# Kernel optimization log

Measured on AMD Instinct MI355X. Metric: run time of the kernel, lower is better.

Reference implementation:

```python
import jax, jax.numpy as jnp
import numpy as np

NUM_CLASSES = 10
PGD_NUMS = 10
ALPHA = 0.15
# Hardcoded in the original module: sign vector for 10 classes
SIGN_VEC = jnp.array([-1.0] * 4 + [1.0] * 6, dtype=jnp.float32)


def setup_inputs() -> dict:
    key = jax.random.key(0)
    k1, k2, k3 = jax.random.split(key, 3)
    B = 1048576
    logit = jax.random.normal(k1, (B, NUM_CLASSES), dtype=jnp.float32)
    y = jax.random.randint(k2, (B,), 0, NUM_CLASSES, dtype=jnp.int32)
    label_freq = jax.random.randint(k3, (NUM_CLASSES,), 0, PGD_NUMS, dtype=jnp.int32)
    return {"logit": logit, "y": y, "label_freq": label_freq}


def _compute_adv(logit, y):
    # softmax over classes, then per-class mean of softmax rows (one-hot^T @ p)
    p = jax.nn.softmax(logit, axis=-1)  # [B, C]
    sum_class_logit = jax.ops.segment_sum(p, y, num_segments=NUM_CLASSES)  # [C, C]
    counts = jax.ops.segment_sum(jnp.ones(y.shape[0], dtype=logit.dtype), y,
                                 num_segments=NUM_CLASSES)  # [C]
    counts = jnp.where(counts == 0, jnp.asarray(100.0, logit.dtype), counts)
    mean_class_logit = sum_class_logit / counts[:, None]  # [C, C]
    grad = mean_class_logit - jnp.eye(NUM_CLASSES, dtype=logit.dtype)
    # Faithful to torch: norm over dim=0 (columns), then reshape(-1,1) divides row i
    col_norm = jnp.linalg.norm(grad, axis=0)  # [C]
    grad = grad / col_norm[:, None]
    grad = ALPHA * grad * SIGN_VEC[:, None].astype(logit.dtype)
    return grad[y]  # index_select along dim 0 -> [B, C]


def reference(logit, y, label_freq):
    logit_copy = logit

    def step(l, _):
        l_new = l + _compute_adv(l, y)
        return l_new, l_new

    _, logit_steps = jax.lax.scan(step, logit, None, length=PGD_NUMS)  # [P, B, C]

    # Original: logit_news = sum_i logit_steps[label_freq[i]] * (y == i)
    # Since class masks are disjoint, this is a per-sample gather of step label_freq[y[n]].
    steps_per_sample = label_freq[y]  # [B]
    B = logit.shape[0]
    logit_news = logit_steps[steps_per_sample, jnp.arange(B)]  # [B, C]

    # mean cross-entropy
    log_p = jax.nn.log_softmax(logit_news, axis=-1)
    loss_adv = -jnp.mean(jnp.take_along_axis(log_p, y[:, None].astype(jnp.int32), axis=1))
    return loss_adv, logit_news, logit_copy
```

## Files before the change

### kernel.cpp

```cpp
#include <hip/hip_runtime.h>

#define PGD   10
#define ALPHA 0.15f
#define NTAB  32
#define NTHR  256
#define SPT   4
#define FTHR  256
#define FSPT  4

#define WS_COUNTS 0
#define WS_STAB   320
#define WS_DGLOB  32320
#define WS_ZERO_N 33320

__global__ void k_init(float* __restrict__ ws, float* __restrict__ out) {
    int i = blockIdx.x * blockDim.x + threadIdx.x;
    if (i == 0) out[0] = 0.f;
    int gs = gridDim.x * blockDim.x;
    for (int k = i; k < WS_ZERO_N; k += gs) ws[k] = 0.f;
}

__device__ __forceinline__ void load4(const float* __restrict__ logit,
                                      const int* __restrict__ y,
                                      int s0, int B, float a[40], int yc[4]) {
    if (s0 + 4 <= B) {
        const float4* rp = reinterpret_cast<const float4*>(logit + (size_t)s0 * 10);
        float4 q[10];
        #pragma unroll
        for (int i = 0; i < 10; ++i) q[i] = rp[i];
        int4 yv = *reinterpret_cast<const int4*>(y + s0);
        #pragma unroll
        for (int i = 0; i < 10; ++i) {
            a[4 * i + 0] = q[i].x; a[4 * i + 1] = q[i].y;
            a[4 * i + 2] = q[i].z; a[4 * i + 3] = q[i].w;
        }
        yc[0] = yv.x; yc[1] = yv.y; yc[2] = yv.z; yc[3] = yv.w;
    } else {
        #pragma unroll
        for (int k = 0; k < 4; ++k) {
            int idx = s0 + k;
            if (idx < B) {
                yc[k] = y[idx];
                for (int j = 0; j < 10; ++j) a[k * 10 + j] = logit[(size_t)idx * 10 + j];
            } else {
                yc[k] = -1;
                for (int j = 0; j < 10; ++j) a[k * 10 + j] = 0.f;
            }
        }
    }
}

__global__ __launch_bounds__(NTHR) void k_step(
    const float* __restrict__ logit, const int* __restrict__ y,
    float* __restrict__ ws, int B, int t )
{
    __shared__ float sh_D[100];
    __shared__ float shT[100];
    __shared__ float shCnt[10];
    __shared__ float shCn[10];
    __shared__ float wtab[8][100];
    __shared__ float ctab[8][10];

    const int tid = threadIdx.x;

    float* counts_tab = ws + WS_COUNTS;
    float* S_tab      = ws + WS_STAB;
    float* D_glob     = ws + WS_DGLOB;

    for (int i = tid; i < 800; i += NTHR) (&wtab[0][0])[i] = 0.f;
    if (t == 1) for (int i = tid; i < 80; i += NTHR) (&ctab[0][0])[i] = 0.f;

    if (t >= 2) {
        const float* Sg = S_tab + (size_t)(t - 2) * (NTAB * 100);
        if (tid < 10) {
            float s = 0.f;
            #pragma unroll
            for (int k = 0; k < NTAB; ++k) s += counts_tab[k * 10 + tid];
            shCnt[tid] = (s == 0.f) ? 100.f : s;
        }
        if (tid < 100) {
            float s = 0.f;
            #pragma unroll
            for (int k = 0; k < NTAB; ++k) s += Sg[k * 100 + tid];
            shT[tid] = s;
        }
        __syncthreads();
        if (tid < 100) {
            int c = tid / 10, j = tid - c * 10;
            shT[tid] = shT[tid] / shCnt[c] - ((c == j) ? 1.f : 0.f);
        }
        __syncthreads();
        if (tid < 10) {
            float s = 0.f;
            for (int cc = 0; cc < 10; ++cc) { float g = shT[cc * 10 + tid]; s += g * g; }
            shCn[tid] = sqrtf(s);
        }
        __syncthreads();
        if (tid < 100) {
            int c = tid / 10;
            float sign = (c < 4) ? -1.f : 1.f;
            float g = shT[tid] / shCn[c] * (ALPHA * sign);
            sh_D[tid] = ((t >= 3) ? D_glob[(size_t)(t - 3) * 100 + tid] : 0.f) + g;
        }
        __syncthreads();
        if (blockIdx.x == 0 && tid < 100) D_glob[(size_t)(t - 2) * 100 + tid] = sh_D[tid];
    }
    __syncthreads();

    const int s0 = (blockIdx.x * NTHR + tid) * SPT;
    float a[40];
    int   yc[4];
    load4(logit, y, s0, B, a, yc);

    const int sub = ((tid >> 6) << 1) | (tid & 1);
    #pragma unroll
    for (int k = 0; k < SPT; ++k) {
        int c = yc[k];
        if (c < 0) continue;
        float tv[10];
        #pragma unroll
        for (int j = 0; j < 10; ++j) tv[j] = a[k * 10 + j];
        if (t >= 2) {
            #pragma unroll
            for (int j = 0; j < 10; ++j) tv[j] += sh_D[c * 10 + j];
        }
        float m = tv[0];
        #pragma unroll
        for (int j = 1; j < 10; ++j) m = fmaxf(m, tv[j]);
        float s = 0.f;
        #pragma unroll
        for (int j = 0; j < 10; ++j) { tv[j] = __expf(tv[j] - m); s += tv[j]; }
        float r = 1.f / s;
        #pragma unroll
        for (int j = 0; j < 10; ++j) unsafeAtomicAdd(&wtab[sub][c * 10 + j], tv[j] * r);
        if (t == 1) unsafeAtomicAdd(&ctab[sub][c], 1.f);
    }
    __syncthreads();

    const int tb = blockIdx.x & (NTAB - 1);
    if (tid < 100) {
        float s = 0.f;
        #pragma unroll
        for (int w = 0; w < 8; ++w) s += wtab[w][tid];
        unsafeAtomicAdd(&S_tab[(size_t)(t - 1) * (NTAB * 100) + (size_t)tb * 100 + tid], s);
    }
    if (t == 1 && tid < 10) {
        float s = 0.f;
        #pragma unroll
        for (int w = 0; w < 8; ++w) s += ctab[w][tid];
        unsafeAtomicAdd(&counts_tab[tb * 10 + tid], s);
    }
}

__global__ __launch_bounds__(FTHR) void k_final(
    const float* __restrict__ logit, const int* __restrict__ y,
    const int* __restrict__ label_freq,
    float* __restrict__ out, float* __restrict__ ws, int B)
{
    __shared__ float Dall[PGD][100];
    __shared__ float shT[100];
    __shared__ float shCnt[10];
    __shared__ float shCn[10];
    __shared__ int   lf[10];
    __shared__ float wsum[4];

    const int tid = threadIdx.x;

    float* counts_tab = ws + WS_COUNTS;
    float* S_tab      = ws + WS_STAB;
    float* D_glob     = ws + WS_DGLOB;

    {
        const float* Sg = S_tab + (size_t)9 * (NTAB * 100);
        if (tid < 10) {
            float s = 0.f;
            #pragma unroll
            for (int k = 0; k < NTAB; ++k) s += counts_tab[k * 10 + tid];
            shCnt[tid] = (s == 0.f) ? 100.f : s;
        }
        if (tid < 100) {
            float s = 0.f;
            #pragma unroll
            for (int k = 0; k < NTAB; ++k) s += Sg[k * 100 + tid];
            shT[tid] = s;
        }
        __syncthreads();
        if (tid < 100) {
            int c = tid / 10, j = tid - c * 10;
            shT[tid] = shT[tid] / shCnt[c] - ((c == j) ? 1.f : 0.f);
        }
        __syncthreads();
        if (tid < 10) {
            float s = 0.f;
            for (int cc = 0; cc < 10; ++cc) { float g = shT[cc * 10 + tid]; s += g * g; }
            shCn[tid] = sqrtf(s);
        }
        __syncthreads();
        if (tid < 100) {
            int c = tid / 10;
            float sign = (c < 4) ? -1.f : 1.f;
            float g = shT[tid] / shCn[c] * (ALPHA * sign);
            Dall[9][tid] = D_glob[8 * 100 + tid] + g;
        }
        for (int i = tid; i < 900; i += FTHR) Dall[i / 100][i % 100] = D_glob[i];
        if (tid < 10) lf[tid] = label_freq[tid];
        __syncthreads();
    }

    const int s0 = (blockIdx.x * FTHR + tid) * FSPT;
    float a[40];
    int   yc[4];
    load4(logit, y, s0, B, a, yc);

    float* news_out = out + 1;
    float* copy_out = out + 1 + (size_t)B * 10;
    float acc = 0.f;
    #pragma unroll
    for (int k = 0; k < FSPT; ++k) {
        int idx = s0 + k;
        if (idx >= B || yc[k] < 0) continue;
        int c = yc[k];
        int sel = lf[c];
        float nv[10];
        #pragma unroll
        for (int j = 0; j < 10; ++j) nv[j] = a[k * 10 + j] + Dall[sel][c * 10 + j];
        float2* np = reinterpret_cast<float2*>(news_out + (size_t)idx * 10);
        float2* cp = reinterpret_cast<float2*>(copy_out + (size_t)idx * 10);
        #pragma unroll
        for (int q = 0; q < 5; ++q) {
            np[q] = make_float2(nv[2 * q], nv[2 * q + 1]);
            cp[q] = make_float2(a[k * 10 + 2 * q], a[k * 10 + 2 * q + 1]);
        }
        float m = nv[0];
        #pragma unroll
        for (int j = 1; j < 10; ++j) m = fmaxf(m, nv[j]);
        float s = 0.f;
        #pragma unroll
        for (int j = 0; j < 10; ++j) s += __expf(nv[j] - m);
        acc += __logf(s) + m - nv[c];
    }
    #pragma unroll
    for (int off = 32; off > 0; off >>= 1) acc += __shfl_down(acc, off);
    if ((tid & 63) == 0) wsum[tid >> 6] = acc;
    __syncthreads();
    if (tid == 0)
        unsafeAtomicAdd(out, (wsum[0] + wsum[1] + wsum[2] + wsum[3]) / (float)B);
}

extern "C" void kernel_launch(void* const* d_in, const int* in_sizes, int n_in,
                              void* d_out, int out_size, void* d_ws, size_t ws_size,
                              hipStream_t stream) {
    const float* logit = (const float*)d_in[0];
    const int*   yy    = (const int*)d_in[1];
    const int*   lf    = (const int*)d_in[2];
    float* out = (float*)d_out;
    float* ws  = (float*)d_ws;
    int B = in_sizes[0] / 10;

    int blocks  = (B + NTHR * SPT - 1) / (NTHR * SPT);
    int fblocks = (B + FTHR * FSPT - 1) / (FTHR * FSPT);

    hipLaunchKernelGGL(k_init, dim3(64), dim3(256), 0, stream, ws, out);
    for (int t = 1; t <= PGD; ++t)
        hipLaunchKernelGGL(k_step, dim3(blocks), dim3(NTHR), 0, stream,
                           logit, yy, ws, B, t);
    hipLaunchKernelGGL(k_final, dim3(fblocks), dim3(FTHR), 0, stream,
                       logit, yy, lf, out, ws, B);
}
```

Before: 670.6 us.

## Stage logit tiles through shared memory for coalesced loads and stores

Each block now loads 1024 samples as fully coalesced float4 reads (thread-strided rather than per-thread contiguous 160-byte chunks) into an LDS tile, then processes samples from shared memory. The final kernel writes the copy and new-logit outputs as coalesced contiguous streams from the tile instead of strided float2 stores. Global loads are issued before the table reduction phase so their latency overlaps that phase. In exchange, each block uses about 45 KB of LDS, which limits occupancy, and adds extra barriers.

```diff
diff --git a/kernel.cpp b/kernel.cpp
--- a/kernel.cpp
+++ b/kernel.cpp
@@ -4,9 +4,8 @@
 #define ALPHA 0.15f
 #define NTAB  32
 #define NTHR  256
-#define SPT   4
-#define FTHR  256
-#define FSPT  4
+#define TSAMP 1024
+#define NSUB  8
 
 #define WS_COUNTS 0
 #define WS_STAB   320
@@ -20,33 +19,69 @@
     for (int k = i; k < WS_ZERO_N; k += gs) ws[k] = 0.f;
 }
 
-__device__ __forceinline__ void load4(const float* __restrict__ logit,
-                                      const int* __restrict__ y,
-                                      int s0, int B, float a[40], int yc[4]) {
-    if (s0 + 4 <= B) {
-        const float4* rp = reinterpret_cast<const float4*>(logit + (size_t)s0 * 10);
-        float4 q[10];
-        #pragma unroll
-        for (int i = 0; i < 10; ++i) q[i] = rp[i];
-        int4 yv = *reinterpret_cast<const int4*>(y + s0);
-        #pragma unroll
-        for (int i = 0; i < 10; ++i) {
-            a[4 * i + 0] = q[i].x; a[4 * i + 1] = q[i].y;
-            a[4 * i + 2] = q[i].z; a[4 * i + 3] = q[i].w;
+__device__ __forceinline__ void table_phase(
+    const float* __restrict__ Sg, const float* __restrict__ counts_tab,
+    const float* __restrict__ Dprev,
+    float* shT, float* shCnt, float* shCn, float* shD_out, int tid)
+{
+    if (tid < 10) {
+        float s = 0.f;
+        #pragma unroll
+        for (int k = 0; k < NTAB; ++k) s += counts_tab[k * 10 + tid];
+        shCnt[tid] = (s == 0.f) ? 100.f : s;
+    }
+    if (tid < 100) {
+        float s = 0.f;
+        #pragma unroll
+        for (int k = 0; k < NTAB; ++k) s += Sg[k * 100 + tid];
+        shT[tid] = s;
+    }
+    __syncthreads();
+    if (tid < 100) {
+        int c = tid / 10, j = tid - c * 10;
+        shT[tid] = shT[tid] / shCnt[c] - ((c == j) ? 1.f : 0.f);
+    }
+    __syncthreads();
+    if (tid < 10) {
+        float s = 0.f;
+        for (int cc = 0; cc < 10; ++cc) { float g = shT[cc * 10 + tid]; s += g * g; }
+        shCn[tid] = sqrtf(s);
+    }
+    __syncthreads();
+    if (tid < 100) {
+        int c = tid / 10;
+        float sign = (c < 4) ? -1.f : 1.f;
+        float g = shT[tid] / shCn[c] * (ALPHA * sign);
+        shD_out[tid] = (Dprev ? Dprev[tid] : 0.f) + g;
+    }
+    __syncthreads();
+}
+
+__device__ __forceinline__ void load_tile(const float* __restrict__ logit,
+                                          const int* __restrict__ y,
+                                          size_t fbase, size_t ftot, int B,
+                                          int tid, int blk, float4 q[10], int4& yq)
+{
+    #pragma unroll
+    for (int i = 0; i < 10; ++i) {
+        size_t fi = fbase + (size_t)(tid + i * NTHR) * 4;
+        if (fi + 4 <= ftot) {
+            q[i] = *reinterpret_cast<const float4*>(logit + fi);
+        } else {
+            float e[4];
+            #pragma unroll
+            for (int e2 = 0; e2 < 4; ++e2) e[e2] = (fi + e2 < ftot) ? logit[fi + e2] : 0.f;
+            q[i] = make_float4(e[0], e[1], e[2], e[3]);
         }
-        yc[0] = yv.x; yc[1] = yv.y; yc[2] = yv.z; yc[3] = yv.w;
+    }
+    int yi = blk * TSAMP + tid * 4;
+    if (yi + 4 <= B) {
+        yq = *reinterpret_cast<const int4*>(y + yi);
     } else {
-        #pragma unroll
-        for (int k = 0; k < 4; ++k) {
-            int idx = s0 + k;
-            if (idx < B) {
-                yc[k] = y[idx];
-                for (int j = 0; j < 10; ++j) a[k * 10 + j] = logit[(size_t)idx * 10 + j];
-            } else {
-                yc[k] = -1;
-                for (int j = 0; j < 10; ++j) a[k * 10 + j] = 0.f;
-            }
-        }
+        yq.x = (yi     < B) ? y[yi]     : 0;
+        yq.y = (yi + 1 < B) ? y[yi + 1] : 0;
+        yq.z = (yi + 2 < B) ? y[yi + 2] : 0;
+        yq.w = (yi + 3 < B) ? y[yi + 3] : 0;
     }
 }
 
@@ -54,12 +89,14 @@
     const float* __restrict__ logit, const int* __restrict__ y,
     float* __restrict__ ws, int B, int t )
 {
+    __shared__ float tile[TSAMP * 10];
+    __shared__ int   yt[TSAMP];
+    __shared__ float wtab[NSUB][100];
+    __shared__ float ctab[NSUB][10];
     __shared__ float sh_D[100];
     __shared__ float shT[100];
     __shared__ float shCnt[10];
     __shared__ float shCn[10];
-    __shared__ float wtab[8][100];
-    __shared__ float ctab[8][10];
 
     const int tid = threadIdx.x;
 
@@ -67,59 +104,39 @@
     float* S_tab      = ws + WS_STAB;
     float* D_glob     = ws + WS_DGLOB;
 
-    for (int i = tid; i < 800; i += NTHR) (&wtab[0][0])[i] = 0.f;
-    if (t == 1) for (int i = tid; i < 80; i += NTHR) (&ctab[0][0])[i] = 0.f;
+    const size_t fbase = (size_t)blockIdx.x * (TSAMP * 10);
+    const size_t ftot  = (size_t)B * 10;
+    float4 q[10];
+    int4 yq;
+    load_tile(logit, y, fbase, ftot, B, tid, blockIdx.x, q, yq);
+
+    for (int i = tid; i < NSUB * 100; i += NTHR) (&wtab[0][0])[i] = 0.f;
+    if (t == 1) for (int i = tid; i < NSUB * 10; i += NTHR) (&ctab[0][0])[i] = 0.f;
 
     if (t >= 2) {
-        const float* Sg = S_tab + (size_t)(t - 2) * (NTAB * 100);
-        if (tid < 10) {
-            float s = 0.f;
-            #pragma unroll
-            for (int k = 0; k < NTAB; ++k) s += counts_tab[k * 10 + tid];
-            shCnt[tid] = (s == 0.f) ? 100.f : s;
-        }
-        if (tid < 100) {
-            float s = 0.f;
-            #pragma unroll
-            for (int k = 0; k < NTAB; ++k) s += Sg[k * 100 + tid];
-            shT[tid] = s;
-        }
-        __syncthreads();
-        if (tid < 100) {
-            int c = tid / 10, j = tid - c * 10;
-            shT[tid] = shT[tid] / shCnt[c] - ((c == j) ? 1.f : 0.f);
-        }
-        __syncthreads();
-        if (tid < 10) {
-            float s = 0.f;
-            for (int cc = 0; cc < 10; ++cc) { float g = shT[cc * 10 + tid]; s += g * g; }
-            shCn[tid] = sqrtf(s);
-        }
-        __syncthreads();
-        if (tid < 100) {
-            int c = tid / 10;
-            float sign = (c < 4) ? -1.f : 1.f;
-            float g = shT[tid] / shCn[c] * (ALPHA * sign);
-            sh_D[tid] = ((t >= 3) ? D_glob[(size_t)(t - 3) * 100 + tid] : 0.f) + g;
-        }
-        __syncthreads();
+        table_phase(S_tab + (size_t)(t - 2) * (NTAB * 100), counts_tab,
+                    (t >= 3) ? (D_glob + (size_t)(t - 3) * 100) : nullptr,
+                    shT, shCnt, shCn, sh_D, tid);
         if (blockIdx.x == 0 && tid < 100) D_glob[(size_t)(t - 2) * 100 + tid] = sh_D[tid];
     }
-    __syncthreads();
-
-    const int s0 = (blockIdx.x * NTHR + tid) * SPT;
-    float a[40];
-    int   yc[4];
-    load4(logit, y, s0, B, a, yc);
+
+    float4* tp = reinterpret_cast<float4*>(tile);
+    #pragma unroll
+    for (int i = 0; i < 10; ++i) tp[tid + i * NTHR] = q[i];
+    reinterpret_cast<int4*>(yt)[tid] = yq;
+    __syncthreads();
 
     const int sub = ((tid >> 6) << 1) | (tid & 1);
     #pragma unroll
-    for (int k = 0; k < SPT; ++k) {
-        int c = yc[k];
-        if (c < 0) continue;
+    for (int k = 0; k < 4; ++k) {
+        int sl = tid + k * NTHR;
+        int gi = blockIdx.x * TSAMP + sl;
+        if (gi >= B) break;
+        int c = yt[sl];
+        const float2* rp = reinterpret_cast<const float2*>(tile + sl * 10);
         float tv[10];
         #pragma unroll
-        for (int j = 0; j < 10; ++j) tv[j] = a[k * 10 + j];
+        for (int h = 0; h < 5; ++h) { float2 v = rp[h]; tv[2 * h] = v.x; tv[2 * h + 1] = v.y; }
         if (t >= 2) {
             #pragma unroll
             for (int j = 0; j < 10; ++j) tv[j] += sh_D[c * 10 + j];
@@ -141,22 +158,24 @@
     if (tid < 100) {
         float s = 0.f;
         #pragma unroll
-        for (int w = 0; w < 8; ++w) s += wtab[w][tid];
+        for (int w = 0; w < NSUB; ++w) s += wtab[w][tid];
         unsafeAtomicAdd(&S_tab[(size_t)(t - 1) * (NTAB * 100) + (size_t)tb * 100 + tid], s);
     }
     if (t == 1 && tid < 10) {
         float s = 0.f;
         #pragma unroll
-        for (int w = 0; w < 8; ++w) s += ctab[w][tid];
+        for (int w = 0; w < NSUB; ++w) s += ctab[w][tid];
         unsafeAtomicAdd(&counts_tab[tb * 10 + tid], s);
     }
 }
 
-__global__ __launch_bounds__(FTHR) void k_final(
+__global__ __launch_bounds__(NTHR) void k_final(
     const float* __restrict__ logit, const int* __restrict__ y,
     const int* __restrict__ label_freq,
     float* __restrict__ out, float* __restrict__ ws, int B)
 {
+    __shared__ float tile[TSAMP * 10];
+    __shared__ int   yt[TSAMP];
     __shared__ float Dall[PGD][100];
     __shared__ float shT[100];
     __shared__ float shCnt[10];
@@ -170,67 +189,49 @@
     float* S_tab      = ws + WS_STAB;
     float* D_glob     = ws + WS_DGLOB;
 
-    {
-        const float* Sg = S_tab + (size_t)9 * (NTAB * 100);
-        if (tid < 10) {
-            float s = 0.f;
-            #pragma unroll
-            for (int k = 0; k < NTAB; ++k) s += counts_tab[k * 10 + tid];
-            shCnt[tid] = (s == 0.f) ? 100.f : s;
+    const size_t fbase = (size_t)blockIdx.x * (TSAMP * 10);
+    const size_t ftot  = (size_t)B * 10;
+    float4 q[10];
+    int4 yq;
+    load_tile(logit, y, fbase, ftot, B, tid, blockIdx.x, q, yq);
+
+    table_phase(S_tab + (size_t)9 * (NTAB * 100), counts_tab, D_glob + 8 * 100,
+                shT, shCnt, shCn, &Dall[9][0], tid);
+    for (int i = tid; i < 900; i += NTHR) Dall[i / 100][i % 100] = D_glob[i];
+    if (tid < 10) lf[tid] = label_freq[tid];
+
+    float4* tp = reinterpret_cast<float4*>(tile);
+    #pragma unroll
+    for (int i = 0; i < 10; ++i) tp[tid + i * NTHR] = q[i];
+    reinterpret_cast<int4*>(yt)[tid] = yq;
+    __syncthreads();
+
+    const int vfloat = (int)((ftot - fbase < (size_t)(TSAMP * 10)) ? (ftot - fbase)
+                                                                   : (size_t)(TSAMP * 10));
+    float* news_out = out + 1;
+    float* copy_out = out + 1 + ftot;
+
+    for (int m = tid; m < vfloat; m += NTHR) copy_out[fbase + m] = tile[m];
+    __syncthreads();
+
+    float acc = 0.f;
+    #pragma unroll
+    for (int k = 0; k < 4; ++k) {
+        int sl = tid + k * NTHR;
+        int gi = blockIdx.x * TSAMP + sl;
+        if (gi >= B) break;
+        int c = yt[sl];
+        int sel = lf[c];
+        float2* rp = reinterpret_cast<float2*>(tile + sl * 10);
+        float nv[10];
+        #pragma unroll
+        for (int h = 0; h < 5; ++h) {
+            float2 v = rp[h];
+            nv[2 * h]     = v.x + Dall[sel][c * 10 + 2 * h];
+            nv[2 * h + 1] = v.y + Dall[sel][c * 10 + 2 * h + 1];
         }
-        if (tid < 100) {
-            float s = 0.f;
-            #pragma unroll
-            for (int k = 0; k < NTAB; ++k) s += Sg[k * 100 + tid];
-            shT[tid] = s;
-        }
-        __syncthreads();
-        if (tid < 100) {
-            int c = tid / 10, j = tid - c * 10;
-            shT[tid] = shT[tid] / shCnt[c] - ((c == j) ? 1.f : 0.f);
-        }
-        __syncthreads();
-        if (tid < 10) {
-            float s = 0.f;
-            for (int cc = 0; cc < 10; ++cc) { float g = shT[cc * 10 + tid]; s += g * g; }
-            shCn[tid] = sqrtf(s);
-        }
-        __syncthreads();
-        if (tid < 100) {
-            int c = tid / 10;
-            float sign = (c < 4) ? -1.f : 1.f;
-            float g = shT[tid] / shCn[c] * (ALPHA * sign);
-            Dall[9][tid] = D_glob[8 * 100 + tid] + g;
-        }
-        for (int i = tid; i < 900; i += FTHR) Dall[i / 100][i % 100] = D_glob[i];
-        if (tid < 10) lf[tid] = label_freq[tid];
-        __syncthreads();
-    }
-
-    const int s0 = (blockIdx.x * FTHR + tid) * FSPT;
-    float a[40];
-    int   yc[4];
-    load4(logit, y, s0, B, a, yc);
-
-    float* news_out = out + 1;
-    float* copy_out = out + 1 + (size_t)B * 10;
-    float acc = 0.f;
-    #pragma unroll
-    for (int k = 0; k < FSPT; ++k) {
-        int idx = s0 + k;
-        if (idx >= B || yc[k] < 0) continue;
-        int c = yc[k];
-        int sel = lf[c];
-        float nv[10];
-        #pragma unroll
-        for (int j = 0; j < 10; ++j) nv[j] = a[k * 10 + j] + Dall[sel][c * 10 + j];
-        float2* np = reinterpret_cast<float2*>(news_out + (size_t)idx * 10);
-        float2* cp = reinterpret_cast<float2*>(copy_out + (size_t)idx * 10);
-        #pragma unroll
-        for (int q = 0; q < 5; ++q) {
-            np[q] = make_float2(nv[2 * q], nv[2 * q + 1]);
-            cp[q] = make_float2(a[k * 10 + 2 * q], a[k * 10 + 2 * q + 1]);
-        }
+        #pragma unroll
+        for (int h = 0; h < 5; ++h) rp[h] = make_float2(nv[2 * h], nv[2 * h + 1]);
         float m = nv[0];
         #pragma unroll
         for (int j = 1; j < 10; ++j) m = fmaxf(m, nv[j]);
@@ -239,6 +240,10 @@
         for (int j = 0; j < 10; ++j) s += __expf(nv[j] - m);
         acc += __logf(s) + m - nv[c];
     }
+    __syncthreads();
+
+    for (int m = tid; m < vfloat; m += NTHR) news_out[fbase + m] = tile[m];
+
     #pragma unroll
     for (int off = 32; off > 0; off >>= 1) acc += __shfl_down(acc, off);
     if ((tid & 63) == 0) wsum[tid >> 6] = acc;
@@ -257,13 +262,12 @@
     float* ws  = (float*)d_ws;
     int B = in_sizes[0] / 10;
 
-    int blocks  = (B + NTHR * SPT - 1) / (NTHR * SPT);
-    int fblocks = (B + FTHR * FSPT - 1) / (FTHR * FSPT);
+    int blocks = (B + TSAMP - 1) / TSAMP;
 
     hipLaunchKernelGGL(k_init, dim3(64), dim3(256), 0, stream, ws, out);
     for (int t = 1; t <= PGD; ++t)
         hipLaunchKernelGGL(k_step, dim3(blocks), dim3(NTHR), 0, stream,
                            logit, yy, ws, B, t);
-    hipLaunchKernelGGL(k_final, dim3(fblocks), dim3(FTHR), 0, stream,
+    hipLaunchKernelGGL(k_final, dim3(blocks), dim3(NTHR), 0, stream,
                        logit, yy, lf, out, ws, B);
 }
```

Measured after the change: 662.8 us. Within noise of the previous version (-1.2%).
